# Performance work log

Hardware: AMD Instinct MI355X
Metric: run time of the kernel (lower is better)

Reference implementation:

```python
import jax, jax.numpy as jnp
import numpy as np

SQRT_2_OVER_PI = 0.7978845608028654

def gelu_new(x):
    # HF 'gelu_new': 0.5*x*(1+tanh(sqrt(2/pi)*(x+0.044715*x^3)))
    return 0.5 * x * (1.0 + jnp.tanh(SQRT_2_OVER_PI * (x + 0.044715 * x * x * x)))

def phm_linear(x, phm_rule, W_left, W_right, bias, n):
    # x: [..., n*p]; phm_rule: [n, n, n]; W_left: [n, p, r]; W_right: [n, r, q]
    # H = sum_i kron(phm_rule[i], W_i), W_i = W_left[i] @ W_right[i]; y = x @ H + b
    p = x.shape[-1] // n
    W = jnp.einsum('ipk,ikq->ipq', W_left, W_right)          # [n, p, q]
    xr = x.reshape(x.shape[:-1] + (n, p))                    # [..., n, p]
    # kron(A,B)[a*p+r, c*q+s] = A[a,c]*B[r,s]
    y = jnp.einsum('...ap,iac,ipq->...cq', xr, phm_rule, W)  # [..., n, q]
    y = y.reshape(x.shape[:-1] + (n * W.shape[-1],))
    return y + bias

def setup_inputs() -> dict:
    key = jax.random.key(0)
    ks = jax.random.split(key, 7)
    B, S, D, d, n = 8, 4096, 768, 192, 4
    x = jax.random.normal(ks[0], (B, S, D), dtype=jnp.float32)
    phm_rule_d = jax.random.normal(ks[1], (n, n, n), dtype=jnp.float32) * 0.01
    W_left_d = jax.random.normal(ks[2], (n, D // n, 1), dtype=jnp.float32) * 0.05
    W_right_d = jax.random.normal(ks[3], (n, 1, d // n), dtype=jnp.float32) * 0.05
    bias_d = jnp.zeros((d,), dtype=jnp.float32)
    phm_rule_u = jax.random.normal(ks[4], (n, n, n), dtype=jnp.float32) * 0.01
    W_left_u = jax.random.normal(ks[5], (n, d // n, 1), dtype=jnp.float32) * 0.05
    W_right_u = jax.random.normal(ks[6], (n, 1, D // n), dtype=jnp.float32) * 0.05
    bias_u = jnp.zeros((D,), dtype=jnp.float32)
    return {"x": x, "phm_rule_d": phm_rule_d, "W_left_d": W_left_d, "W_right_d": W_right_d,
            "bias_d": bias_d, "phm_rule_u": phm_rule_u, "W_left_u": W_left_u,
            "W_right_u": W_right_u, "bias_u": bias_u}

def reference(x, phm_rule_d, W_left_d, W_right_d, bias_d, phm_rule_u, W_left_u, W_right_u, bias_u):
    n = phm_rule_d.shape[0]
    z = phm_linear(x, phm_rule_d, W_left_d, W_right_d, bias_d, n)
    z = gelu_new(z)
    return phm_linear(z, phm_rule_u, W_left_u, W_right_u, bias_u, n)
```

## Files before the change

kernel.cpp:

```cpp
#include <hip/hip_runtime.h>
#include <math.h>


#define SQ2PI 0.79788456080286535588f
#define T_TILE 8

__global__ __launch_bounds__(256, 4)
void phm_fused(const float* __restrict__ x,
               const float* __restrict__ rule_d,
               const float* __restrict__ Wl_d,
               const float* __restrict__ Wr_d,
               const float* __restrict__ bias_d,
               const float* __restrict__ rule_u,
               const float* __restrict__ Wl_u,
               const float* __restrict__ Wr_u,
               const float* __restrict__ bias_u,
               float* __restrict__ out,
               int n_tokens)
{
    __shared__ __attribute__((aligned(16))) float sTile[T_TILE * 768];
    __shared__ __attribute__((aligned(16))) float sLd[768];
    __shared__ __attribute__((aligned(16))) float sLu[192];
    __shared__ __attribute__((aligned(16))) float sRu[768];
    __shared__ float sRuleD[64];
    __shared__ float sRuleU[64];

    const int tid = threadIdx.x;
    for (int i = tid; i < 768; i += 256) sLd[i] = Wl_d[i];
    for (int i = tid; i < 192; i += 256) sLu[i] = Wl_u[i];
    for (int i = tid; i < 768; i += 256) sRu[i] = Wr_u[i];
    if (tid < 64)       sRuleD[tid]      = rule_d[tid];
    else if (tid < 128) sRuleU[tid - 64] = rule_u[tid - 64];

    const int lane = tid & 63;
    const int wave = tid >> 6;
    const int a    = lane >> 4;
    const int r    = lane & 15;

    float bd[3];
    float rdw[4][3];
    float4 bu[3];
    #pragma unroll
    for (int w = 0; w < 3; ++w) bd[w] = bias_d[a*48 + 3*r + w];
    #pragma unroll
    for (int i = 0; i < 4; ++i)
        #pragma unroll
        for (int w = 0; w < 3; ++w) rdw[i][w] = Wr_d[i*48 + 3*r + w];
    #pragma unroll
    for (int u = 0; u < 3; ++u)
        bu[u] = *(const float4*)(bias_u + a*192 + 12*r + 4*u);
    __syncthreads();

    const long long total4 = (long long)n_tokens * 192;
    const int n_tiles = (n_tokens + T_TILE - 1) / T_TILE;

    for (int tile = blockIdx.x; tile < n_tiles; tile += gridDim.x) {
        const long long g4 = (long long)tile * (T_TILE * 192);

        #pragma unroll
        for (int j = 0; j < (T_TILE * 192) / 256; ++j) {
            const int idx = tid + j * 256;
            const long long gi = g4 + idx;
            float4 v = make_float4(0.f, 0.f, 0.f, 0.f);
            if (gi < total4) v = *(const float4*)(x + gi * 4);
            *(float4*)&sTile[idx * 4] = v;
        }
        __syncthreads();

        #pragma unroll
        for (int s = 0; s < T_TILE / 4; ++s) {
            const int tloc = wave * (T_TILE / 4) + s;
            const int tok  = tile * T_TILE + tloc;
            if (tok < n_tokens) {
                float* xt = &sTile[tloc * 768 + a * 192 + 12 * r];
                float4 xv[3];
                #pragma unroll
                for (int u = 0; u < 3; ++u) xv[u] = *(const float4*)(xt + 4 * u);

                float sd[4] = {0.f, 0.f, 0.f, 0.f};
                #pragma unroll
                for (int u = 0; u < 3; ++u) {
                    #pragma unroll
                    for (int i = 0; i < 4; ++i) {
                        const float4 lv = *(const float4*)(&sLd[i*192 + 12*r + 4*u]);
                        sd[i] = fmaf(xv[u].x, lv.x, sd[i]);
                        sd[i] = fmaf(xv[u].y, lv.y, sd[i]);
                        sd[i] = fmaf(xv[u].z, lv.z, sd[i]);
                        sd[i] = fmaf(xv[u].w, lv.w, sd[i]);
                    }
                }
                #pragma unroll
                for (int i = 0; i < 4; ++i)
                    #pragma unroll
                    for (int off = 1; off < 16; off <<= 1)
                        sd[i] += __shfl_xor(sd[i], off);

                float sA[4][4];
                #pragma unroll
                for (int aa = 0; aa < 4; ++aa)
                    #pragma unroll
                    for (int i = 0; i < 4; ++i)
                        sA[i][aa] = __shfl(sd[i], aa*16 + r);

                float tD[4];
                #pragma unroll
                for (int i = 0; i < 4; ++i) {
                    float acc = 0.f;
                    #pragma unroll
                    for (int aa = 0; aa < 4; ++aa)
                        acc = fmaf(sA[i][aa], sRuleD[i*16 + aa*4 + a], acc);
                    tD[i] = acc;
                }

                float g[3];
                #pragma unroll
                for (int w = 0; w < 3; ++w) {
                    float z = bd[w];
                    #pragma unroll
                    for (int i = 0; i < 4; ++i) z = fmaf(tD[i], rdw[i][w], z);
                    const float inner = SQ2PI * fmaf(0.044715f*z, z*z, z);
                    const float e  = __expf(2.0f*inner);
                    const float th = 1.0f - 2.0f/(e + 1.0f);
                    g[w] = 0.5f*z*(1.0f + th);
                }

                float p[4] = {0.f, 0.f, 0.f, 0.f};
                #pragma unroll
                for (int w = 0; w < 3; ++w) {
                    const int q = 3*r + w;
                    #pragma unroll
                    for (int i = 0; i < 4; ++i)
                        p[i] = fmaf(g[w], sLu[i*48 + q], p[i]);
                }
                #pragma unroll
                for (int i = 0; i < 4; ++i)
                    #pragma unroll
                    for (int off = 1; off < 16; off <<= 1)
                        p[i] += __shfl_xor(p[i], off);

                float sA2[4][4];
                #pragma unroll
                for (int aa = 0; aa < 4; ++aa)
                    #pragma unroll
                    for (int i = 0; i < 4; ++i)
                        sA2[i][aa] = __shfl(p[i], aa*16 + r);

                float tU[4];
                #pragma unroll
                for (int i = 0; i < 4; ++i) {
                    float acc = 0.f;
                    #pragma unroll
                    for (int aa = 0; aa < 4; ++aa)
                        acc = fmaf(sA2[i][aa], sRuleU[i*16 + aa*4 + a], acc);
                    tU[i] = acc;
                }

                #pragma unroll
                for (int u = 0; u < 3; ++u) {
                    float4 ov = bu[u];
                    #pragma unroll
                    for (int i = 0; i < 4; ++i) {
                        const float4 ru = *(const float4*)(&sRu[i*192 + 12*r + 4*u]);
                        ov.x = fmaf(tU[i], ru.x, ov.x);
                        ov.y = fmaf(tU[i], ru.y, ov.y);
                        ov.z = fmaf(tU[i], ru.z, ov.z);
                        ov.w = fmaf(tU[i], ru.w, ov.w);
                    }
                    *(float4*)(xt + 4 * u) = ov;
                }
            }
        }
        __syncthreads();

        #pragma unroll
        for (int j = 0; j < (T_TILE * 192) / 256; ++j) {
            const int idx = tid + j * 256;
            const long long gi = g4 + idx;
            if (gi < total4)
                *(float4*)(out + gi * 4) = *(const float4*)&sTile[idx * 4];
        }
        __syncthreads();
    }
}

extern "C" void kernel_launch(void* const* d_in, const int* in_sizes, int n_in,
                              void* d_out, int out_size, void* d_ws, size_t ws_size,
                              hipStream_t stream) {
    const float* x      = (const float*)d_in[0];
    const float* rule_d = (const float*)d_in[1];
    const float* Wl_d   = (const float*)d_in[2];
    const float* Wr_d   = (const float*)d_in[3];
    const float* bias_d = (const float*)d_in[4];
    const float* rule_u = (const float*)d_in[5];
    const float* Wl_u   = (const float*)d_in[6];
    const float* Wr_u   = (const float*)d_in[7];
    const float* bias_u = (const float*)d_in[8];
    float* out          = (float*)d_out;

    const int n_tokens = in_sizes[0] / 768;

    phm_fused<<<dim3(1024), dim3(256), 0, stream>>>(
        x, rule_d, Wl_d, Wr_d, bias_d, rule_u, Wl_u, Wr_u, bias_u, out, n_tokens);
}
```

Baseline: 205.1 us.

## Keep PHM weights in registers and use DPP row-rotate reductions

Moves the down-projection left weights, up-projection left weights and both rule tensors from LDS into per-thread registers, precomputing the rule coefficients permuted by lane xor. Replaces the shfl_xor butterfly within 16 lanes with DPP row_ror adds, and swaps the 16 generic shuffles for 3 xor shuffles per component. The aim is to cut LDS traffic and ds_bpermute shuffle cost. In exchange it uses more VGPRs, so launch bounds drop from 4 to 3 blocks per CU.

```diff
diff --git a/kernel.cpp b/kernel.cpp
--- a/kernel.cpp
+++ b/kernel.cpp
@@ -5,7 +5,20 @@
 #define SQ2PI 0.79788456080286535588f
 #define T_TILE 8
 
-__global__ __launch_bounds__(256, 4)
+template<int CTRL>
+__device__ __forceinline__ float ror_add(float v) {
+    int s = __builtin_amdgcn_update_dpp(0, __float_as_int(v), CTRL, 0xF, 0xF, true);
+    return v + __int_as_float(s);
+}
+__device__ __forceinline__ float reduce16(float v) {
+    v = ror_add<0x121>(v);
+    v = ror_add<0x122>(v);
+    v = ror_add<0x124>(v);
+    v = ror_add<0x128>(v);
+    return v;
+}
+
+__global__ __launch_bounds__(256, 3)
 void phm_fused(const float* __restrict__ x,
                const float* __restrict__ rule_d,
                const float* __restrict__ Wl_d,
@@ -19,24 +32,38 @@
                int n_tokens)
 {
     __shared__ __attribute__((aligned(16))) float sTile[T_TILE * 768];
-    __shared__ __attribute__((aligned(16))) float sLd[768];
-    __shared__ __attribute__((aligned(16))) float sLu[192];
     __shared__ __attribute__((aligned(16))) float sRu[768];
-    __shared__ float sRuleD[64];
-    __shared__ float sRuleU[64];
 
     const int tid = threadIdx.x;
-    for (int i = tid; i < 768; i += 256) sLd[i] = Wl_d[i];
-    for (int i = tid; i < 192; i += 256) sLu[i] = Wl_u[i];
     for (int i = tid; i < 768; i += 256) sRu[i] = Wr_u[i];
-    if (tid < 64)       sRuleD[tid]      = rule_d[tid];
-    else if (tid < 128) sRuleU[tid - 64] = rule_u[tid - 64];
 
     const int lane = tid & 63;
     const int wave = tid >> 6;
     const int a    = lane >> 4;
     const int r    = lane & 15;
 
+    float4 ld[4][3];
+    #pragma unroll
+    for (int i = 0; i < 4; ++i)
+        #pragma unroll
+        for (int u = 0; u < 3; ++u)
+            ld[i][u] = *(const float4*)(Wl_d + i*192 + 12*r + 4*u);
+
+    float lu[4][3];
+    #pragma unroll
+    for (int i = 0; i < 4; ++i)
+        #pragma unroll
+        for (int w = 0; w < 3; ++w) lu[i][w] = Wl_u[i*48 + 3*r + w];
+
+    float rD[4][4], rU[4][4];
+    #pragma unroll
+    for (int k = 0; k < 4; ++k)
+        #pragma unroll
+        for (int i = 0; i < 4; ++i) {
+            rD[k][i] = rule_d[i*16 + (a^k)*4 + a];
+            rU[k][i] = rule_u[i*16 + (a^k)*4 + a];
+        }
+
     float bd[3];
     float rdw[4][3];
     float4 bu[3];
@@ -49,6 +76,7 @@
     #pragma unroll
     for (int u = 0; u < 3; ++u)
         bu[u] = *(const float4*)(bias_u + a*192 + 12*r + 4*u);
+
     __syncthreads();
 
     const long long total4 = (long long)n_tokens * 192;
@@ -77,39 +105,30 @@
                 #pragma unroll
                 for (int u = 0; u < 3; ++u) xv[u] = *(const float4*)(xt + 4 * u);
 
-                float sd[4] = {0.f, 0.f, 0.f, 0.f};
-                #pragma unroll
-                for (int u = 0; u < 3; ++u) {
-                    #pragma unroll
-                    for (int i = 0; i < 4; ++i) {
-                        const float4 lv = *(const float4*)(&sLd[i*192 + 12*r + 4*u]);
-                        sd[i] = fmaf(xv[u].x, lv.x, sd[i]);
-                        sd[i] = fmaf(xv[u].y, lv.y, sd[i]);
-                        sd[i] = fmaf(xv[u].z, lv.z, sd[i]);
-                        sd[i] = fmaf(xv[u].w, lv.w, sd[i]);
-                    }
-                }
-                #pragma unroll
-                for (int i = 0; i < 4; ++i)
-                    #pragma unroll
-                    for (int off = 1; off < 16; off <<= 1)
-                        sd[i] += __shfl_xor(sd[i], off);
-
-                float sA[4][4];
-                #pragma unroll
-                for (int aa = 0; aa < 4; ++aa)
-                    #pragma unroll
-                    for (int i = 0; i < 4; ++i)
-                        sA[i][aa] = __shfl(sd[i], aa*16 + r);
-
-                float tD[4];
+                float sd[4];
                 #pragma unroll
                 for (int i = 0; i < 4; ++i) {
                     float acc = 0.f;
                     #pragma unroll
-                    for (int aa = 0; aa < 4; ++aa)
-                        acc = fmaf(sA[i][aa], sRuleD[i*16 + aa*4 + a], acc);
-                    tD[i] = acc;
+                    for (int u = 0; u < 3; ++u) {
+                        acc = fmaf(xv[u].x, ld[i][u].x, acc);
+                        acc = fmaf(xv[u].y, ld[i][u].y, acc);
+                        acc = fmaf(xv[u].z, ld[i][u].z, acc);
+                        acc = fmaf(xv[u].w, ld[i][u].w, acc);
+                    }
+                    sd[i] = reduce16(acc);
+                }
+
+                float tD[4];
+                #pragma unroll
+                for (int i = 0; i < 4; ++i) {
+                    const float x1 = __shfl_xor(sd[i], 16);
+                    const float x2 = __shfl_xor(sd[i], 32);
+                    const float x3 = __shfl_xor(x1,    32);
+                    tD[i] = fmaf(sd[i], rD[0][i],
+                            fmaf(x1,   rD[1][i],
+                            fmaf(x2,   rD[2][i],
+                                 x3 *  rD[3][i])));
                 }
 
                 float g[3];
@@ -124,35 +143,20 @@
                     g[w] = 0.5f*z*(1.0f + th);
                 }
 
-                float p[4] = {0.f, 0.f, 0.f, 0.f};
-                #pragma unroll
-                for (int w = 0; w < 3; ++w) {
-                    const int q = 3*r + w;
-                    #pragma unroll
-                    for (int i = 0; i < 4; ++i)
-                        p[i] = fmaf(g[w], sLu[i*48 + q], p[i]);
-                }
-                #pragma unroll
-                for (int i = 0; i < 4; ++i)
-                    #pragma unroll
-                    for (int off = 1; off < 16; off <<= 1)
-                        p[i] += __shfl_xor(p[i], off);
-
-                float sA2[4][4];
-                #pragma unroll
-                for (int aa = 0; aa < 4; ++aa)
-                    #pragma unroll
-                    for (int i = 0; i < 4; ++i)
-                        sA2[i][aa] = __shfl(p[i], aa*16 + r);
-
                 float tU[4];
                 #pragma unroll
                 for (int i = 0; i < 4; ++i) {
                     float acc = 0.f;
                     #pragma unroll
-                    for (int aa = 0; aa < 4; ++aa)
-                        acc = fmaf(sA2[i][aa], sRuleU[i*16 + aa*4 + a], acc);
-                    tU[i] = acc;
+                    for (int w = 0; w < 3; ++w) acc = fmaf(g[w], lu[i][w], acc);
+                    const float h  = reduce16(acc);
+                    const float x1 = __shfl_xor(h,  16);
+                    const float x2 = __shfl_xor(h,  32);
+                    const float x3 = __shfl_xor(x1, 32);
+                    tU[i] = fmaf(h,  rU[0][i],
+                            fmaf(x1, rU[1][i],
+                            fmaf(x2, rU[2][i],
+                                 x3 * rU[3][i])));
                 }
 
                 #pragma unroll
```

Result: slower. 260.5 us (+27.1%).
